# Performance work log

Measured on AMD Instinct MI355X. Metric: run time of the kernel, lower is better.

## Reference

```python
import jax, jax.numpy as jnp
import numpy as np

BIG_NEG = -1000000000.0
B, N, X, D = 16, 32, 36, 2048
H = 512

def setup_inputs() -> dict:
    key = jax.random.key(0)
    ks = jax.random.split(key, 16)
    inp = {
        'fc_feats_target': jax.random.normal(ks[0], (B, 1, D), jnp.float32),
        'fc_feats_distr': jax.random.normal(ks[1], (B, N, D), jnp.float32),
        'att_feats_target': jax.random.normal(ks[2], (B, 1, X, D), jnp.float32),
        'att_feats_distr': jax.random.normal(ks[3], (B, N, X, D), jnp.float32),
        'att_masks_target': jax.random.randint(ks[4], (B, 1, X), 0, 2, jnp.int32),
        'att_masks_distr': jax.random.randint(ks[5], (B, N, X), 0, 2, jnp.int32),
        # scorer MLP params: Linear(2D->H), Linear(H->1)
        'W1': jax.random.normal(ks[6], (2 * D, H), jnp.float32) * 0.02,
        'b1': jnp.zeros((H,), jnp.float32),
        'W2': jax.random.normal(ks[7], (H, 1), jnp.float32) * 0.02,
        'b2': jnp.zeros((1,), jnp.float32),
        # bilinear weight, initialized to identity as in the module
        'Wbil': jnp.eye(D, dtype=jnp.float32),
        # object_scorer MLP params
        'oW1': jax.random.normal(ks[8], (2 * D, H), jnp.float32) * 0.02,
        'ob1': jnp.zeros((H,), jnp.float32),
        'oW2': jax.random.normal(ks[9], (H, 1), jnp.float32) * 0.02,
        'ob2': jnp.zeros((1,), jnp.float32),
    }
    return inp

def _mlp(x, W1, b1, W2, b2):
    h = jax.nn.relu(x @ W1 + b1)
    return (h @ W2 + b2)[..., 0]  # squeeze(-1)

def reference(fc_feats_target, fc_feats_distr, att_feats_target, att_feats_distr,
              att_masks_target, att_masks_distr,
              W1, b1, W2, b2, Wbil, oW1, ob1, oW2, ob2):
    # base scorer on global (fc) features
    ft = jnp.broadcast_to(fc_feats_target, fc_feats_distr.shape)  # [B,N,D]
    cat_feats = jnp.concatenate([ft, fc_feats_distr], axis=-1)    # [B,N,2D]
    scores = _mlp(cat_feats, W1, b1, W2, b2)                      # [B,N]

    # bilinear compatibility: einsum('bixd,biye,de->bixy') with target broadcast over i
    tproj = jnp.einsum('bxd,de->bxe', att_feats_target[:, 0], Wbil)        # [B,X,D]
    inners = jnp.einsum('bxd,biyd->bixy', tproj, att_feats_distr)          # [B,N,X,Y]

    mask_outer = (att_masks_target[:, 0][:, None, :, None]
                  * att_masks_distr[:, :, None, :])                        # [B,N,X,Y]
    inners = jnp.where(mask_outer > 0, inners, BIG_NEG)

    target_weights = jax.nn.softmax(jnp.max(inners, axis=3), axis=-1)      # [B,N,X]
    distr_weights = jax.nn.softmax(jnp.max(inners, axis=2), axis=-1)       # [B,N,Y]

    target_feats = jnp.einsum('bxd,bix->bid', att_feats_target[:, 0], target_weights)
    distr_feats = jnp.einsum('biyd,biy->bid', att_feats_distr, distr_weights)

    cat_att = jnp.concatenate([target_feats, distr_feats], axis=-1)        # [B,N,2D]
    scores = scores + _mlp(cat_att, oW1, ob1, oW2, ob2)

    return jax.nn.log_softmax(scores, axis=-1)  # [B,N]
```

## Files before the change

### kernel.cpp

```cpp
#include <hip/hip_runtime.h>
#include <math.h>

#define D_   2048
#define H_   512
#define K2D  4096
#define X_   36
#define NCOL 1152

#define Z_MLP 16
#define Z_TP  4
#define Z_S   2

#define O_A   0u
#define O_B   4718592u
#define O_TW  6815744u
#define O_DW  6834176u
#define O_SB  6852608u
#define O_SO  6853120u

#define SP_PLANE 663552u

typedef __attribute__((ext_vector_type(8))) short bf8_t;
typedef __attribute__((ext_vector_type(4))) float f4_t;

__device__ __forceinline__ unsigned short f2bf(float f) {
  unsigned u = __float_as_uint(f);
  unsigned r = u + 0x7FFFu + ((u >> 16) & 1u);
  return (unsigned short)(r >> 16);
}
__device__ __forceinline__ float bf2f(unsigned short h) {
  return __uint_as_float(((unsigned)h) << 16);
}

#define TSTR 40

__global__ __launch_bounds__(256, 1) void gemm_mfma(
    const float* __restrict__ A, const float* __restrict__ A2,
    const float* __restrict__ Bm, float* __restrict__ Cpart,
    int M, int N, int K, int kchunk, int amode)
{
  __shared__ __align__(16) unsigned short AsH[128 * TSTR], AsL[128 * TSTR];
  __shared__ __align__(16) unsigned short BsH[128 * TSTR], BsL[128 * TSTR];
  const int t  = threadIdx.x;
  const int m0 = blockIdx.y << 7;
  const int n0 = blockIdx.x << 7;
  const int k0 = blockIdx.z * kchunk;
  const int kend = k0 + kchunk;
  const int w  = t >> 6;
  const int ln = t & 15;
  const int qd = (t >> 4) & 3;
  const int wm = (w >> 1) << 6;
  const int wn = (w & 1) << 6;

  f4_t acc[4][4];
  #pragma unroll
  for (int i = 0; i < 4; i++)
    #pragma unroll
    for (int j = 0; j < 4; j++) acc[i][j] = (f4_t)0.f;

  for (int kb = k0; kb < kend; kb += 32) {
    __syncthreads();
    if (t < 128) {
      int col = t;
      float v[32];
      #pragma unroll
      for (int k = 0; k < 32; k++)
        v[k] = Bm[(size_t)(kb + k) * N + n0 + col];
      __align__(16) unsigned short hb[32], lb[32];
      #pragma unroll
      for (int k = 0; k < 32; k++) {
        unsigned short h = f2bf(v[k]);
        hb[k] = h;
        lb[k] = f2bf(v[k] - bf2f(h));
      }
      #pragma unroll
      for (int j = 0; j < 4; j++) {
        *(bf8_t*)&BsH[col * TSTR + j * 8] = *(bf8_t*)&hb[j * 8];
        *(bf8_t*)&BsL[col * TSTR + j * 8] = *(bf8_t*)&lb[j * 8];
      }
    } else {
      int row = t - 128;
      int gr  = m0 + row;
      float4 va[8];
      #pragma unroll
      for (int j = 0; j < 8; j++) va[j] = make_float4(0.f, 0.f, 0.f, 0.f);
      if (gr < M) {
        #pragma unroll
        for (int j = 0; j < 8; j++) {
          int gk = kb + (j << 2);
          const float* src;
          if (amode == 0) src = A + (size_t)gr * K + gk;
          else src = (gk < 2048) ? (A  + ((size_t)(gr >> 5) << 11) + gk)
                                 : (A2 + ((size_t)gr << 11) + (gk - 2048));
          va[j] = *(const float4*)src;
        }
      }
      __align__(16) unsigned short hb[32], lb[32];
      #pragma unroll
      for (int j = 0; j < 8; j++) {
        float x0 = va[j].x, x1 = va[j].y, x2 = va[j].z, x3 = va[j].w;
        unsigned short h0 = f2bf(x0), h1 = f2bf(x1), h2 = f2bf(x2), h3 = f2bf(x3);
        hb[4*j+0] = h0; hb[4*j+1] = h1; hb[4*j+2] = h2; hb[4*j+3] = h3;
        lb[4*j+0] = f2bf(x0 - bf2f(h0));
        lb[4*j+1] = f2bf(x1 - bf2f(h1));
        lb[4*j+2] = f2bf(x2 - bf2f(h2));
        lb[4*j+3] = f2bf(x3 - bf2f(h3));
      }
      #pragma unroll
      for (int j = 0; j < 4; j++) {
        *(bf8_t*)&AsH[row * TSTR + j * 8] = *(bf8_t*)&hb[j * 8];
        *(bf8_t*)&AsL[row * TSTR + j * 8] = *(bf8_t*)&lb[j * 8];
      }
    }
    __syncthreads();
    bf8_t ah[4], al[4], bh[4], bl[4];
    #pragma unroll
    for (int fm = 0; fm < 4; fm++) {
      int r = (wm + (fm << 4) + ln) * TSTR + (qd << 3);
      ah[fm] = *(const bf8_t*)&AsH[r];
      al[fm] = *(const bf8_t*)&AsL[r];
    }
    #pragma unroll
    for (int fn = 0; fn < 4; fn++) {
      int r = (wn + (fn << 4) + ln) * TSTR + (qd << 3);
      bh[fn] = *(const bf8_t*)&BsH[r];
      bl[fn] = *(const bf8_t*)&BsL[r];
    }
    #pragma unroll
    for (int fm = 0; fm < 4; fm++)
      #pragma unroll
      for (int fn = 0; fn < 4; fn++) {
        acc[fm][fn] = __builtin_amdgcn_mfma_f32_16x16x32_bf16(ah[fm], bh[fn], acc[fm][fn], 0, 0, 0);
        acc[fm][fn] = __builtin_amdgcn_mfma_f32_16x16x32_bf16(ah[fm], bl[fn], acc[fm][fn], 0, 0, 0);
        acc[fm][fn] = __builtin_amdgcn_mfma_f32_16x16x32_bf16(al[fm], bh[fn], acc[fm][fn], 0, 0, 0);
      }
  }
  float* Cz = Cpart + (size_t)blockIdx.z * M * N;
  #pragma unroll
  for (int fm = 0; fm < 4; fm++) {
    #pragma unroll
    for (int reg = 0; reg < 4; reg++) {
      int gr = m0 + wm + (fm << 4) + (qd << 2) + reg;
      if (gr < M) {
        #pragma unroll
        for (int fn = 0; fn < 4; fn++)
          Cz[(size_t)gr * N + n0 + wn + (fn << 4) + ln] = acc[fm][fn][reg];
      }
    }
  }
}

__global__ __launch_bounds__(256) void reduce_tp(
    const float* __restrict__ tpp, float* __restrict__ tproj)
{
  int idx = blockIdx.x * 256 + threadIdx.x;
  const float4* p = (const float4*)tpp;
  float4 a = p[idx];
  #pragma unroll
  for (int z = 1; z < Z_TP; z++) {
    float4 b = p[idx + (size_t)z * 294912];
    a.x += b.x; a.y += b.y; a.z += b.z; a.w += b.w;
  }
  ((float4*)tproj)[idx] = a;
}

__global__ __launch_bounds__(256, 1) void sgemm36_mfma(
    const float* __restrict__ tproj, const float* __restrict__ attd,
    float* __restrict__ Spart, int kchunk)
{
  __shared__ __align__(16) unsigned short AsH[48 * TSTR], AsL[48 * TSTR];
  __shared__ __align__(16) unsigned short BsH[128 * TSTR], BsL[128 * TSTR];
  const int t  = threadIdx.x;
  const int n0 = blockIdx.x << 7;
  const int b  = blockIdx.y;
  const int k0 = blockIdx.z * kchunk;
  const int kend = k0 + kchunk;
  const int w  = t >> 6;
  const int ln = t & 15;
  const int qd = (t >> 4) & 3;
  const float* Ab = tproj + (size_t)b * X_ * D_;
  const float* Bb = attd  + (size_t)b * NCOL * D_;

  f4_t acc[3][2];
  #pragma unroll
  for (int i = 0; i < 3; i++)
    #pragma unroll
    for (int j = 0; j < 2; j++) acc[i][j] = (f4_t)0.f;

  for (int kb = k0; kb < kend; kb += 32) {
    __syncthreads();
    if (t < 128) {
      int col = t;
      float4 v[8];
      #pragma unroll
      for (int j = 0; j < 8; j++)
        v[j] = *(const float4*)(Bb + (size_t)(n0 + col) * D_ + kb + (j << 2));
      __align__(16) unsigned short hb[32], lb[32];
      #pragma unroll
      for (int j = 0; j < 8; j++) {
        float x0 = v[j].x, x1 = v[j].y, x2 = v[j].z, x3 = v[j].w;
        unsigned short h0 = f2bf(x0), h1 = f2bf(x1), h2 = f2bf(x2), h3 = f2bf(x3);
        hb[4*j+0] = h0; hb[4*j+1] = h1; hb[4*j+2] = h2; hb[4*j+3] = h3;
        lb[4*j+0] = f2bf(x0 - bf2f(h0));
        lb[4*j+1] = f2bf(x1 - bf2f(h1));
        lb[4*j+2] = f2bf(x2 - bf2f(h2));
        lb[4*j+3] = f2bf(x3 - bf2f(h3));
      }
      #pragma unroll
      for (int j = 0; j < 4; j++) {
        *(bf8_t*)&BsH[col * TSTR + j * 8] = *(bf8_t*)&hb[j * 8];
        *(bf8_t*)&BsL[col * TSTR + j * 8] = *(bf8_t*)&lb[j * 8];
      }
    } else if (t < 176) {
      int row = t - 128;
      float4 v[8];
      #pragma unroll
      for (int j = 0; j < 8; j++) v[j] = make_float4(0.f, 0.f, 0.f, 0.f);
      if (row < X_) {
        #pragma unroll
        for (int j = 0; j < 8; j++)
          v[j] = *(const float4*)(Ab + (size_t)row * D_ + kb + (j << 2));
      }
      __align__(16) unsigned short hb[32], lb[32];
      #pragma unroll
      for (int j = 0; j < 8; j++) {
        float x0 = v[j].x, x1 = v[j].y, x2 = v[j].z, x3 = v[j].w;
        unsigned short h0 = f2bf(x0), h1 = f2bf(x1), h2 = f2bf(x2), h3 = f2bf(x3);
        hb[4*j+0] = h0; hb[4*j+1] = h1; hb[4*j+2] = h2; hb[4*j+3] = h3;
        lb[4*j+0] = f2bf(x0 - bf2f(h0));
        lb[4*j+1] = f2bf(x1 - bf2f(h1));
        lb[4*j+2] = f2bf(x2 - bf2f(h2));
        lb[4*j+3] = f2bf(x3 - bf2f(h3));
      }
      #pragma unroll
      for (int j = 0; j < 4; j++) {
        *(bf8_t*)&AsH[row * TSTR + j * 8] = *(bf8_t*)&hb[j * 8];
        *(bf8_t*)&AsL[row * TSTR + j * 8] = *(bf8_t*)&lb[j * 8];
      }
    }
    __syncthreads();
    bf8_t ah[3], al[3], bh[2], bl[2];
    #pragma unroll
    for (int fm = 0; fm < 3; fm++) {
      int r = ((fm << 4) + ln) * TSTR + (qd << 3);
      ah[fm] = *(const bf8_t*)&AsH[r];
      al[fm] = *(const bf8_t*)&AsL[r];
    }
    #pragma unroll
    for (int fn = 0; fn < 2; fn++) {
      int r = ((w << 5) + (fn << 4) + ln) * TSTR + (qd << 3);
      bh[fn] = *(const bf8_t*)&BsH[r];
      bl[fn] = *(const bf8_t*)&BsL[r];
    }
    #pragma unroll
    for (int fm = 0; fm < 3; fm++)
      #pragma unroll
      for (int fn = 0; fn < 2; fn++) {
        acc[fm][fn] = __builtin_amdgcn_mfma_f32_16x16x32_bf16(ah[fm], bh[fn], acc[fm][fn], 0, 0, 0);
        acc[fm][fn] = __builtin_amdgcn_mfma_f32_16x16x32_bf16(ah[fm], bl[fn], acc[fm][fn], 0, 0, 0);
        acc[fm][fn] = __builtin_amdgcn_mfma_f32_16x16x32_bf16(al[fm], bh[fn], acc[fm][fn], 0, 0, 0);
      }
  }
  float* Sz = Spart + (size_t)blockIdx.z * SP_PLANE + (size_t)b * X_ * NCOL;
  #pragma unroll
  for (int fm = 0; fm < 3; fm++) {
    #pragma unroll
    for (int reg = 0; reg < 4; reg++) {
      int x = (fm << 4) + (qd << 2) + reg;
      if (x < X_) {
        #pragma unroll
        for (int fn = 0; fn < 2; fn++) {
          int col = n0 + (w << 5) + (fn << 4) + ln;
          Sz[(size_t)x * NCOL + col] = acc[fm][fn][reg];
        }
      }
    }
  }
}

__global__ __launch_bounds__(256) void mlp_tail_z(
    const float* __restrict__ hp, const float* __restrict__ b1,
    const float* __restrict__ w2, const float* __restrict__ b2,
    float* __restrict__ out)
{
  int row = blockIdx.x;
  int t   = threadIdx.x;
  float v = 0.f;
  #pragma unroll
  for (int q = 0; q < 2; q++) {
    int h = t + (q << 8);
    float s = 0.f;
    #pragma unroll
    for (int z = 0; z < Z_MLP; z++)
      s += hp[(size_t)z * (H_ * 512) + (size_t)row * H_ + h];
    s += b1[h];
    v += fmaxf(s, 0.f) * w2[h];
  }
  #pragma unroll
  for (int off = 32; off > 0; off >>= 1) v += __shfl_down(v, off, 64);
  __shared__ float red[4];
  if ((t & 63) == 0) red[t >> 6] = v;
  __syncthreads();
  if (t == 0) out[row] = red[0] + red[1] + red[2] + red[3] + b2[0];
}

__global__ __launch_bounds__(64) void attn_weights(
    const float* __restrict__ Spart, const int* __restrict__ amt,
    const int* __restrict__ amd, float* __restrict__ tw, float* __restrict__ dw)
{
  __shared__ float Sm[36 * 37];
  __shared__ int   mtv[36], mdv[36];
  __shared__ float mrow[36], mcol[36];
  int bi = blockIdx.x;
  int b  = bi >> 5;
  int i  = bi & 31;
  int t  = threadIdx.x;
  if (t < 36) { mtv[t] = amt[b * 36 + t]; mdv[t] = amd[bi * 36 + t]; }
  __syncthreads();
  for (int f = t; f < 324; f += 64) {
    int x  = f / 9;
    int yq = (f - x * 9) << 2;
    size_t o = (((size_t)b * X_ + x) * NCOL + i * 36 + yq) >> 2;
    const float4* p = (const float4*)Spart;
    float4 v = p[o];
    #pragma unroll
    for (int z = 1; z < Z_S; z++) {
      float4 w2 = p[o + ((size_t)z * SP_PLANE >> 2)];
      v.x += w2.x; v.y += w2.y; v.z += w2.z; v.w += w2.w;
    }
    float* dst = &Sm[x * 37 + yq];
    bool mx = (mtv[x] != 0);
    dst[0] = (mx && mdv[yq + 0] != 0) ? v.x : -1e9f;
    dst[1] = (mx && mdv[yq + 1] != 0) ? v.y : -1e9f;
    dst[2] = (mx && mdv[yq + 2] != 0) ? v.z : -1e9f;
    dst[3] = (mx && mdv[yq + 3] != 0) ? v.w : -1e9f;
  }
  __syncthreads();
  if (t < 36) {
    float r = -INFINITY, c = -INFINITY;
    for (int k = 0; k < 36; k++) {
      r = fmaxf(r, Sm[t * 37 + k]);
      c = fmaxf(c, Sm[k * 37 + t]);
    }
    mrow[t] = r; mcol[t] = c;
  }
  __syncthreads();
  {
    float v = (t < 36) ? mrow[t] : -INFINITY;
    float m = v;
    #pragma unroll
    for (int off = 32; off > 0; off >>= 1) m = fmaxf(m, __shfl_xor(m, off, 64));
    float e = (t < 36) ? expf(v - m) : 0.f;
    float s = e;
    #pragma unroll
    for (int off = 32; off > 0; off >>= 1) s += __shfl_xor(s, off, 64);
    if (t < 36) tw[bi * 36 + t] = e / s;
  }
  {
    float v = (t < 36) ? mcol[t] : -INFINITY;
    float m = v;
    #pragma unroll
    for (int off = 32; off > 0; off >>= 1) m = fmaxf(m, __shfl_xor(m, off, 64));
    float e = (t < 36) ? expf(v - m) : 0.f;
    float s = e;
    #pragma unroll
    for (int off = 32; off > 0; off >>= 1) s += __shfl_xor(s, off, 64);
    if (t < 36) dw[bi * 36 + t] = e / s;
  }
}

__global__ __launch_bounds__(256) void wfeats(
    const float* __restrict__ attt, const float* __restrict__ attd,
    const float* __restrict__ tw, const float* __restrict__ dw,
    float* __restrict__ cat)
{
  __shared__ float twl[36], dwl[36];
  int bi = blockIdx.x, b = bi >> 5, t = threadIdx.x;
  if (t < 36) { twl[t] = tw[bi * 36 + t]; dwl[t] = dw[bi * 36 + t]; }
  __syncthreads();
  const float4* at4 = (const float4*)(attt + (size_t)b * X_ * D_);
  const float4* ad4 = (const float4*)(attd + (size_t)bi * X_ * D_);
  float4 t0 = make_float4(0, 0, 0, 0), t1 = t0, d0 = t0, d1 = t0;
  for (int x = 0; x < 36; x++) {
    float wt = twl[x], wd = dwl[x];
    float4 a  = at4[x * 512 + t];
    float4 a2 = at4[x * 512 + t + 256];
    float4 e  = ad4[x * 512 + t];
    float4 e2 = ad4[x * 512 + t + 256];
    t0.x = fmaf(wt, a.x, t0.x);  t0.y = fmaf(wt, a.y, t0.y);
    t0.z = fmaf(wt, a.z, t0.z);  t0.w = fmaf(wt, a.w, t0.w);
    t1.x = fmaf(wt, a2.x, t1.x); t1.y = fmaf(wt, a2.y, t1.y);
    t1.z = fmaf(wt, a2.z, t1.z); t1.w = fmaf(wt, a2.w, t1.w);
    d0.x = fmaf(wd, e.x, d0.x);  d0.y = fmaf(wd, e.y, d0.y);
    d0.z = fmaf(wd, e.z, d0.z);  d0.w = fmaf(wd, e.w, d0.w);
    d1.x = fmaf(wd, e2.x, d1.x); d1.y = fmaf(wd, e2.y, d1.y);
    d1.z = fmaf(wd, e2.z, d1.z); d1.w = fmaf(wd, e2.w, d1.w);
  }
  float4* c4 = (float4*)(cat + (size_t)bi * K2D);
  c4[t] = t0; c4[t + 256] = t1; c4[512 + t] = d0; c4[512 + t + 256] = d1;
}

__global__ __launch_bounds__(64) void lsm(
    const float* __restrict__ sb, const float* __restrict__ so,
    float* __restrict__ out)
{
  int b = blockIdx.x, t = threadIdx.x;
  float s = (t < 32) ? sb[b * 32 + t] + so[b * 32 + t] : -INFINITY;
  float m = s;
  #pragma unroll
  for (int off = 32; off > 0; off >>= 1) m = fmaxf(m, __shfl_xor(m, off, 64));
  float e = (t < 32) ? expf(s - m) : 0.f;
  float sum = e;
  #pragma unroll
  for (int off = 32; off > 0; off >>= 1) sum += __shfl_xor(sum, off, 64);
  if (t < 32) out[b * 32 + t] = s - m - logf(sum);
}

extern "C" void kernel_launch(void* const* d_in, const int* in_sizes, int n_in,
                              void* d_out, int out_size, void* d_ws, size_t ws_size,
                              hipStream_t stream)
{
  const float* fc_t  = (const float*)d_in[0];
  const float* fc_d  = (const float*)d_in[1];
  const float* att_t = (const float*)d_in[2];
  const float* att_d = (const float*)d_in[3];
  const int*   am_t  = (const int*)d_in[4];
  const int*   am_d  = (const int*)d_in[5];
  const float* W1    = (const float*)d_in[6];
  const float* b1    = (const float*)d_in[7];
  const float* W2    = (const float*)d_in[8];
  const float* b2    = (const float*)d_in[9];
  const float* Wbil  = (const float*)d_in[10];
  const float* oW1   = (const float*)d_in[11];
  const float* ob1   = (const float*)d_in[12];
  const float* oW2   = (const float*)d_in[13];
  const float* ob2   = (const float*)d_in[14];
  float* ws  = (float*)d_ws;
  float* out = (float*)d_out;

  gemm_mfma<<<dim3(4, 4, Z_MLP), 256, 0, stream>>>(fc_t, fc_d, W1, ws + O_A,
                                                   512, 512, 4096, 4096 / Z_MLP, 1);
  mlp_tail_z<<<512, 256, 0, stream>>>(ws + O_A, b1, W2, b2, ws + O_SB);
  gemm_mfma<<<dim3(16, 5, Z_TP), 256, 0, stream>>>(att_t, nullptr, Wbil, ws + O_A,
                                                   576, 2048, 2048, 2048 / Z_TP, 0);
  reduce_tp<<<1152, 256, 0, stream>>>(ws + O_A, ws + O_B);
  sgemm36_mfma<<<dim3(9, 16, Z_S), 256, 0, stream>>>(ws + O_B, att_d, ws + O_A,
                                                     2048 / Z_S);
  attn_weights<<<512, 64, 0, stream>>>(ws + O_A, am_t, am_d, ws + O_TW, ws + O_DW);
  wfeats<<<512, 256, 0, stream>>>(att_t, att_d, ws + O_TW, ws + O_DW, ws + O_B);
  gemm_mfma<<<dim3(4, 4, Z_MLP), 256, 0, stream>>>(ws + O_B, nullptr, oW1, ws + O_A,
                                                   512, 512, 4096, 4096 / Z_MLP, 0);
  mlp_tail_z<<<512, 256, 0, stream>>>(ws + O_A, ob1, oW2, ob2, ws + O_SO);
  lsm<<<16, 64, 0, stream>>>(ws + O_SB, ws + O_SO, out);
}
```

Before: 416.5 us.

## Shrink GEMM tiles, raise split-K, prefetch next tile, fuse attention weights with feature pooling

```diff
diff --git a/kernel.cpp b/kernel.cpp
--- a/kernel.cpp
+++ b/kernel.cpp
@@ -7,16 +7,14 @@
 #define X_   36
 #define NCOL 1152
 
-#define Z_MLP 16
-#define Z_TP  4
-#define Z_S   2
+#define Z_MLP 32
+#define Z_TP  8
+#define Z_S   4
 
 #define O_A   0u
-#define O_B   4718592u
-#define O_TW  6815744u
-#define O_DW  6834176u
-#define O_SB  6852608u
-#define O_SO  6853120u
+#define O_B   9437184u
+#define O_SB  11534336u
+#define O_SO  11534848u
 
 #define SP_PLANE 663552u
 
@@ -34,102 +32,97 @@
 
 #define TSTR 40
 
-__global__ __launch_bounds__(256, 1) void gemm_mfma(
+__device__ __forceinline__ void cvt8(unsigned short* Hp, unsigned short* Lp,
+                                     float4 a, float4 b) {
+  __align__(16) unsigned short h[8], l[8];
+  float x[8] = {a.x, a.y, a.z, a.w, b.x, b.y, b.z, b.w};
+  #pragma unroll
+  for (int j = 0; j < 8; j++) {
+    h[j] = f2bf(x[j]);
+    l[j] = f2bf(x[j] - bf2f(h[j]));
+  }
+  *(bf8_t*)Hp = *(bf8_t*)&h[0];
+  *(bf8_t*)Lp = *(bf8_t*)&l[0];
+}
+
+__global__ __launch_bounds__(256, 4) void gemm_mfma64(
     const float* __restrict__ A, const float* __restrict__ A2,
     const float* __restrict__ Bm, float* __restrict__ Cpart,
     int M, int N, int K, int kchunk, int amode)
 {
-  __shared__ __align__(16) unsigned short AsH[128 * TSTR], AsL[128 * TSTR];
-  __shared__ __align__(16) unsigned short BsH[128 * TSTR], BsL[128 * TSTR];
+  __shared__ __align__(16) unsigned short AsH[64 * TSTR], AsL[64 * TSTR];
+  __shared__ __align__(16) unsigned short BsH[64 * TSTR], BsL[64 * TSTR];
   const int t  = threadIdx.x;
-  const int m0 = blockIdx.y << 7;
-  const int n0 = blockIdx.x << 7;
+  const int m0 = blockIdx.y << 6;
+  const int n0 = blockIdx.x << 6;
   const int k0 = blockIdx.z * kchunk;
   const int kend = k0 + kchunk;
   const int w  = t >> 6;
   const int ln = t & 15;
   const int qd = (t >> 4) & 3;
-  const int wm = (w >> 1) << 6;
-  const int wn = (w & 1) << 6;
-
-  f4_t acc[4][4];
-  #pragma unroll
-  for (int i = 0; i < 4; i++)
-    #pragma unroll
-    for (int j = 0; j < 4; j++) acc[i][j] = (f4_t)0.f;
+  const int wm = (w >> 1) << 5;
+  const int wn = (w & 1) << 5;
+  const int a_row = t >> 2;
+  const int a_kq  = (t & 3) << 3;
+  const int b_col = t & 63;
+  const int b_kq  = (t >> 6) << 3;
+
+  f4_t acc[2][2];
+  #pragma unroll
+  for (int i = 0; i < 2; i++)
+    #pragma unroll
+    for (int j = 0; j < 2; j++) acc[i][j] = (f4_t)0.f;
+
+  float4 pa0, pa1;
+  float  pb[8];
+
+  auto loadA = [&](int kb) {
+    int gr = m0 + a_row;
+    int gk = kb + a_kq;
+    pa0 = make_float4(0.f, 0.f, 0.f, 0.f);
+    pa1 = pa0;
+    if (gr < M) {
+      const float* src;
+      if (amode == 0) src = A + (size_t)gr * K + gk;
+      else src = (gk < 2048) ? (A  + ((size_t)(gr >> 5) << 11) + gk)
+                             : (A2 + ((size_t)gr << 11) + (gk - 2048));
+      pa0 = *(const float4*)src;
+      pa1 = *(const float4*)(src + 4);
+    }
+  };
+  auto loadB = [&](int kb) {
+    #pragma unroll
+    for (int j = 0; j < 8; j++)
+      pb[j] = Bm[(size_t)(kb + b_kq + j) * N + n0 + b_col];
+  };
+
+  loadA(k0); loadB(k0);
 
   for (int kb = k0; kb < kend; kb += 32) {
     __syncthreads();
-    if (t < 128) {
-      int col = t;
-      float v[32];
-      #pragma unroll
-      for (int k = 0; k < 32; k++)
-        v[k] = Bm[(size_t)(kb + k) * N + n0 + col];
-      __align__(16) unsigned short hb[32], lb[32];
-      #pragma unroll
-      for (int k = 0; k < 32; k++) {
-        unsigned short h = f2bf(v[k]);
-        hb[k] = h;
-        lb[k] = f2bf(v[k] - bf2f(h));
-      }
-      #pragma unroll
-      for (int j = 0; j < 4; j++) {
-        *(bf8_t*)&BsH[col * TSTR + j * 8] = *(bf8_t*)&hb[j * 8];
-        *(bf8_t*)&BsL[col * TSTR + j * 8] = *(bf8_t*)&lb[j * 8];
-      }
-    } else {
-      int row = t - 128;
-      int gr  = m0 + row;
-      float4 va[8];
-      #pragma unroll
-      for (int j = 0; j < 8; j++) va[j] = make_float4(0.f, 0.f, 0.f, 0.f);
-      if (gr < M) {
-        #pragma unroll
-        for (int j = 0; j < 8; j++) {
-          int gk = kb + (j << 2);
-          const float* src;
-          if (amode == 0) src = A + (size_t)gr * K + gk;
-          else src = (gk < 2048) ? (A  + ((size_t)(gr >> 5) << 11) + gk)
-                                 : (A2 + ((size_t)gr << 11) + (gk - 2048));
-          va[j] = *(const float4*)src;
-        }
-      }
-      __align__(16) unsigned short hb[32], lb[32];
-      #pragma unroll
-      for (int j = 0; j < 8; j++) {
-        float x0 = va[j].x, x1 = va[j].y, x2 = va[j].z, x3 = va[j].w;
-        unsigned short h0 = f2bf(x0), h1 = f2bf(x1), h2 = f2bf(x2), h3 = f2bf(x3);
-        hb[4*j+0] = h0; hb[4*j+1] = h1; hb[4*j+2] = h2; hb[4*j+3] = h3;
-        lb[4*j+0] = f2bf(x0 - bf2f(h0));
-        lb[4*j+1] = f2bf(x1 - bf2f(h1));
-        lb[4*j+2] = f2bf(x2 - bf2f(h2));
-        lb[4*j+3] = f2bf(x3 - bf2f(h3));
-      }
-      #pragma unroll
-      for (int j = 0; j < 4; j++) {
-        *(bf8_t*)&AsH[row * TSTR + j * 8] = *(bf8_t*)&hb[j * 8];
-        *(bf8_t*)&AsL[row * TSTR + j * 8] = *(bf8_t*)&lb[j * 8];
-      }
-    }
+    cvt8(&AsH[a_row * TSTR + a_kq], &AsL[a_row * TSTR + a_kq], pa0, pa1);
+    cvt8(&BsH[b_col * TSTR + b_kq], &BsL[b_col * TSTR + b_kq],
+         make_float4(pb[0], pb[1], pb[2], pb[3]),
+         make_float4(pb[4], pb[5], pb[6], pb[7]));
     __syncthreads();
-    bf8_t ah[4], al[4], bh[4], bl[4];
-    #pragma unroll
-    for (int fm = 0; fm < 4; fm++) {
+    if (kb + 32 < kend) { loadA(kb + 32); loadB(kb + 32); }
+    bf8_t ah[2], al[2], bh[2], bl[2];
+    #pragma unroll
+    for (int fm = 0; fm < 2; fm++) {
       int r = (wm + (fm << 4) + ln) * TSTR + (qd << 3);
       ah[fm] = *(const bf8_t*)&AsH[r];
       al[fm] = *(const bf8_t*)&AsL[r];
     }
     #pragma unroll
-    for (int fn = 0; fn < 4; fn++) {
+    for (int fn = 0; fn < 2; fn++) {
       int r = (wn + (fn << 4) + ln) * TSTR + (qd << 3);
       bh[fn] = *(const bf8_t*)&BsH[r];
       bl[fn] = *(const bf8_t*)&BsL[r];
     }
     #pragma unroll
-    for (int fm = 0; fm < 4; fm++)
+    for (int fm = 0; fm < 2; fm++)
       #pragma unroll
-      for (int fn = 0; fn < 4; fn++) {
+      for (int fn = 0; fn < 2; fn++) {
         acc[fm][fn] = __builtin_amdgcn_mfma_f32_16x16x32_bf16(ah[fm], bh[fn], acc[fm][fn], 0, 0, 0);
         acc[fm][fn] = __builtin_amdgcn_mfma_f32_16x16x32_bf16(ah[fm], bl[fn], acc[fm][fn], 0, 0, 0);
         acc[fm][fn] = __builtin_amdgcn_mfma_f32_16x16x32_bf16(al[fm], bh[fn], acc[fm][fn], 0, 0, 0);
@@ -137,13 +130,13 @@
   }
   float* Cz = Cpart + (size_t)blockIdx.z * M * N;
   #pragma unroll
-  for (int fm = 0; fm < 4; fm++) {
+  for (int fm = 0; fm < 2; fm++) {
     #pragma unroll
     for (int reg = 0; reg < 4; reg++) {
       int gr = m0 + wm + (fm << 4) + (qd << 2) + reg;
       if (gr < M) {
         #pragma unroll
-        for (int fn = 0; fn < 4; fn++)
+        for (int fn = 0; fn < 2; fn++)
           Cz[(size_t)gr * N + n0 + wn + (fn << 4) + ln] = acc[fm][fn][reg];
       }
     }
@@ -164,14 +157,14 @@
   ((float4*)tproj)[idx] = a;
 }
 
-__global__ __launch_bounds__(256, 1) void sgemm36_mfma(
+__global__ __launch_bounds__(256, 4) void sgemm36_mfma(
     const float* __restrict__ tproj, const float* __restrict__ attd,
     float* __restrict__ Spart, int kchunk)
 {
   __shared__ __align__(16) unsigned short AsH[48 * TSTR], AsL[48 * TSTR];
-  __shared__ __align__(16) unsigned short BsH[128 * TSTR], BsL[128 * TSTR];
+  __shared__ __align__(16) unsigned short BsH[64 * TSTR], BsL[64 * TSTR];
   const int t  = threadIdx.x;
-  const int n0 = blockIdx.x << 7;
+  const int n0 = blockIdx.x << 6;
   const int b  = blockIdx.y;
   const int k0 = blockIdx.z * kchunk;
   const int kend = k0 + kchunk;
@@ -180,86 +173,59 @@
   const int qd = (t >> 4) & 3;
   const float* Ab = tproj + (size_t)b * X_ * D_;
   const float* Bb = attd  + (size_t)b * NCOL * D_;
-
-  f4_t acc[3][2];
-  #pragma unroll
-  for (int i = 0; i < 3; i++)
-    #pragma unroll
-    for (int j = 0; j < 2; j++) acc[i][j] = (f4_t)0.f;
+  const int a_row = t >> 2;
+  const int a_kq  = (t & 3) << 3;
+  const int b_col = t & 63;
+  const int b_kq  = (t >> 6) << 3;
+
+  f4_t acc[3];
+  #pragma unroll
+  for (int i = 0; i < 3; i++) acc[i] = (f4_t)0.f;
+
+  float4 pa0, pa1, pb0, pb1;
+
+  auto loadA = [&](int kb) {
+    pa0 = make_float4(0.f, 0.f, 0.f, 0.f);
+    pa1 = pa0;
+    if (a_row < X_) {
+      const float* src = Ab + (size_t)a_row * D_ + kb + a_kq;
+      pa0 = *(const float4*)src;
+      pa1 = *(const float4*)(src + 4);
+    }
+  };
+  auto loadB = [&](int kb) {
+    const float* src = Bb + (size_t)(n0 + b_col) * D_ + kb + b_kq;
+    pb0 = *(const float4*)src;
+    pb1 = *(const float4*)(src + 4);
+  };
+
+  loadA(k0); loadB(k0);
 
   for (int kb = k0; kb < kend; kb += 32) {
     __syncthreads();
-    if (t < 128) {
-      int col = t;
-      float4 v[8];
-      #pragma unroll
-      for (int j = 0; j < 8; j++)
-        v[j] = *(const float4*)(Bb + (size_t)(n0 + col) * D_ + kb + (j << 2));
-      __align__(16) unsigned short hb[32], lb[32];
-      #pragma unroll
-      for (int j = 0; j < 8; j++) {
-        float x0 = v[j].x, x1 = v[j].y, x2 = v[j].z, x3 = v[j].w;
-        unsigned short h0 = f2bf(x0), h1 = f2bf(x1), h2 = f2bf(x2), h3 = f2bf(x3);
-        hb[4*j+0] = h0; hb[4*j+1] = h1; hb[4*j+2] = h2; hb[4*j+3] = h3;
-        lb[4*j+0] = f2bf(x0 - bf2f(h0));
-        lb[4*j+1] = f2bf(x1 - bf2f(h1));
-        lb[4*j+2] = f2bf(x2 - bf2f(h2));
-        lb[4*j+3] = f2bf(x3 - bf2f(h3));
-      }
-      #pragma unroll
-      for (int j = 0; j < 4; j++) {
-        *(bf8_t*)&BsH[col * TSTR + j * 8] = *(bf8_t*)&hb[j * 8];
-        *(bf8_t*)&BsL[col * TSTR + j * 8] = *(bf8_t*)&lb[j * 8];
-      }
-    } else if (t < 176) {
-      int row = t - 128;
-      float4 v[8];
-      #pragma unroll
-      for (int j = 0; j < 8; j++) v[j] = make_float4(0.f, 0.f, 0.f, 0.f);
-      if (row < X_) {
-        #pragma unroll
-        for (int j = 0; j < 8; j++)
-          v[j] = *(const float4*)(Ab + (size_t)row * D_ + kb + (j << 2));
-      }
-      __align__(16) unsigned short hb[32], lb[32];
-      #pragma unroll
-      for (int j = 0; j < 8; j++) {
-        float x0 = v[j].x, x1 = v[j].y, x2 = v[j].z, x3 = v[j].w;
-        unsigned short h0 = f2bf(x0), h1 = f2bf(x1), h2 = f2bf(x2), h3 = f2bf(x3);
-        hb[4*j+0] = h0; hb[4*j+1] = h1; hb[4*j+2] = h2; hb[4*j+3] = h3;
-        lb[4*j+0] = f2bf(x0 - bf2f(h0));
-        lb[4*j+1] = f2bf(x1 - bf2f(h1));
-        lb[4*j+2] = f2bf(x2 - bf2f(h2));
-        lb[4*j+3] = f2bf(x3 - bf2f(h3));
-      }
-      #pragma unroll
-      for (int j = 0; j < 4; j++) {
-        *(bf8_t*)&AsH[row * TSTR + j * 8] = *(bf8_t*)&hb[j * 8];
-        *(bf8_t*)&AsL[row * TSTR + j * 8] = *(bf8_t*)&lb[j * 8];
-      }
-    }
+    if (a_row < 48)
+      cvt8(&AsH[a_row * TSTR + a_kq], &AsL[a_row * TSTR + a_kq], pa0, pa1);
+    cvt8(&BsH[b_col * TSTR + b_kq], &BsL[b_col * TSTR + b_kq], pb0, pb1);
     __syncthreads();
-    bf8_t ah[3], al[3], bh[2], bl[2];
+    if (kb + 32 < kend) { loadA(kb + 32); loadB(kb + 32); }
+    bf8_t ah[3], al[3], bh, bl;
     #pragma unroll
     for (int fm = 0; fm < 3; fm++) {
       int r = ((fm << 4) + ln) * TSTR + (qd << 3);
       ah[fm] = *(const bf8_t*)&AsH[r];
       al[fm] = *(const bf8_t*)&AsL[r];
     }
-    #pragma unroll
-    for (int fn = 0; fn < 2; fn++) {
-      int r = ((w << 5) + (fn << 4) + ln) * TSTR + (qd << 3);
-      bh[fn] = *(const bf8_t*)&BsH[r];
-      bl[fn] = *(const bf8_t*)&BsL[r];
-    }
-    #pragma unroll
-    for (int fm = 0; fm < 3; fm++)
-      #pragma unroll
-      for (int fn = 0; fn < 2; fn++) {
-        acc[fm][fn] = __builtin_amdgcn_mfma_f32_16x16x32_bf16(ah[fm], bh[fn], acc[fm][fn], 0, 0, 0);
-        acc[fm][fn] = __builtin_amdgcn_mfma_f32_16x16x32_bf16(ah[fm], bl[fn], acc[fm][fn], 0, 0, 0);
-        acc[fm][fn] = __builtin_amdgcn_mfma_f32_16x16x32_bf16(al[fm], bh[fn], acc[fm][fn], 0, 0, 0);
-      }
+    {
+      int r = ((w << 4) + ln) * TSTR + (qd << 3);
+      bh = *(const bf8_t*)&BsH[r];
+      bl = *(const bf8_t*)&BsL[r];
+    }
+    #pragma unroll
+    for (int fm = 0; fm < 3; fm++) {
+      acc[fm] = __builtin_amdgcn_mfma_f32_16x16x32_bf16(ah[fm], bh, acc[fm], 0, 0, 0);
+      acc[fm] = __builtin_amdgcn_mfma_f32_16x16x32_bf16(ah[fm], bl, acc[fm], 0, 0, 0);
+      acc[fm] = __builtin_amdgcn_mfma_f32_16x16x32_bf16(al[fm], bh, acc[fm], 0, 0, 0);
+    }
   }
   float* Sz = Spart + (size_t)blockIdx.z * SP_PLANE + (size_t)b * X_ * NCOL;
   #pragma unroll
@@ -267,13 +233,8 @@
     #pragma unroll
     for (int reg = 0; reg < 4; reg++) {
       int x = (fm << 4) + (qd << 2) + reg;
-      if (x < X_) {
-        #pragma unroll
-        for (int fn = 0; fn < 2; fn++) {
-          int col = n0 + (w << 5) + (fn << 4) + ln;
-          Sz[(size_t)x * NCOL + col] = acc[fm][fn][reg];
-        }
-      }
+      if (x < X_)
+        Sz[(size_t)x * NCOL + n0 + (w << 4) + ln] = acc[fm][reg];
     }
   }
 }
@@ -304,20 +265,21 @@
   if (t == 0) out[row] = red[0] + red[1] + red[2] + red[3] + b2[0];
 }
 
-__global__ __launch_bounds__(64) void attn_weights(
+__global__ __launch_bounds__(256) void attn_fused(
     const float* __restrict__ Spart, const int* __restrict__ amt,
-    const int* __restrict__ amd, float* __restrict__ tw, float* __restrict__ dw)
+    const int* __restrict__ amd, const float* __restrict__ attt,
+    const float* __restrict__ attd, float* __restrict__ cat)
 {
   __shared__ float Sm[36 * 37];
   __shared__ int   mtv[36], mdv[36];
-  __shared__ float mrow[36], mcol[36];
+  __shared__ float mrow[36], mcol[36], twl[36], dwl[36];
   int bi = blockIdx.x;
   int b  = bi >> 5;
   int i  = bi & 31;
   int t  = threadIdx.x;
   if (t < 36) { mtv[t] = amt[b * 36 + t]; mdv[t] = amd[bi * 36 + t]; }
   __syncthreads();
-  for (int f = t; f < 324; f += 64) {
+  for (int f = t; f < 324; f += 256) {
     int x  = f / 9;
     int yq = (f - x * 9) << 2;
     size_t o = (((size_t)b * X_ + x) * NCOL + i * 36 + yq) >> 2;
@@ -325,8 +287,8 @@
     float4 v = p[o];
     #pragma unroll
     for (int z = 1; z < Z_S; z++) {
-      float4 w2 = p[o + ((size_t)z * SP_PLANE >> 2)];
-      v.x += w2.x; v.y += w2.y; v.z += w2.z; v.w += w2.w;
+      float4 wv = p[o + ((size_t)z * SP_PLANE >> 2)];
+      v.x += wv.x; v.y += wv.y; v.z += wv.z; v.w += wv.w;
     }
     float* dst = &Sm[x * 37 + yq];
     bool mx = (mtv[x] != 0);
@@ -345,7 +307,7 @@
     mrow[t] = r; mcol[t] = c;
   }
   __syncthreads();
-  {
+  if (t < 64) {
     float v = (t < 36) ? mrow[t] : -INFINITY;
     float m = v;
     #pragma unroll
@@ -354,29 +316,19 @@
     float s = e;
     #pragma unroll
     for (int off = 32; off > 0; off >>= 1) s += __shfl_xor(s, off, 64);
-    if (t < 36) tw[bi * 36 + t] = e / s;
-  }
-  {
-    float v = (t < 36) ? mcol[t] : -INFINITY;
+    if (t < 36) twl[t] = e / s;
+  } else if (t < 128) {
+    int l = t - 64;
+    float v = (l < 36) ? mcol[l] : -INFINITY;
     float m = v;
     #pragma unroll
     for (int off = 32; off > 0; off >>= 1) m = fmaxf(m, __shfl_xor(m, off, 64));
-    float e = (t < 36) ? expf(v - m) : 0.f;
+    float e = (l < 36) ? expf(v - m) : 0.f;
     float s = e;
     #pragma unroll
     for (int off = 32; off > 0; off >>= 1) s += __shfl_xor(s, off, 64);
-    if (t < 36) dw[bi * 36 + t] = e / s;
-  }
-}
-
-__global__ __launch_bounds__(256) void wfeats(
-    const float* __restrict__ attt, const float* __restrict__ attd,
-    const float* __restrict__ tw, const float* __restrict__ dw,
-    float* __restrict__ cat)
-{
-  __shared__ float twl[36], dwl[36];
-  int bi = blockIdx.x, b = bi >> 5, t = threadIdx.x;
-  if (t < 36) { twl[t] = tw[bi * 36 + t]; dwl[t] = dw[bi * 36 + t]; }
+    if (l < 36) dwl[l] = e / s;
+  }
   __syncthreads();
   const float4* at4 = (const float4*)(attt + (size_t)b * X_ * D_);
   const float4* ad4 = (const float4*)(attd + (size_t)bi * X_ * D_);
@@ -438,18 +390,17 @@
   float* ws  = (float*)d_ws;
   float* out = (float*)d_out;
 
-  gemm_mfma<<<dim3(4, 4, Z_MLP), 256, 0, stream>>>(fc_t, fc_d, W1, ws + O_A,
-                                                   512, 512, 4096, 4096 / Z_MLP, 1);
+  gemm_mfma64<<<dim3(8, 8, Z_MLP), 256, 0, stream>>>(fc_t, fc_d, W1, ws + O_A,
+                                                     512, 512, 4096, 4096 / Z_MLP, 1);
   mlp_tail_z<<<512, 256, 0, stream>>>(ws + O_A, b1, W2, b2, ws + O_SB);
-  gemm_mfma<<<dim3(16, 5, Z_TP), 256, 0, stream>>>(att_t, nullptr, Wbil, ws + O_A,
-                                                   576, 2048, 2048, 2048 / Z_TP, 0);
+  gemm_mfma64<<<dim3(32, 9, Z_TP), 256, 0, stream>>>(att_t, nullptr, Wbil, ws + O_A,
+                                                     576, 2048, 2048, 2048 / Z_TP, 0);
   reduce_tp<<<1152, 256, 0, stream>>>(ws + O_A, ws + O_B);
-  sgemm36_mfma<<<dim3(9, 16, Z_S), 256, 0, stream>>>(ws + O_B, att_d, ws + O_A,
-                                                     2048 / Z_S);
-  attn_weights<<<512, 64, 0, stream>>>(ws + O_A, am_t, am_d, ws + O_TW, ws + O_DW);
-  wfeats<<<512, 256, 0, stream>>>(att_t, att_d, ws + O_TW, ws + O_DW, ws + O_B);
-  gemm_mfma<<<dim3(4, 4, Z_MLP), 256, 0, stream>>>(ws + O_B, nullptr, oW1, ws + O_A,
-                                                   512, 512, 4096, 4096 / Z_MLP, 0);
+  sgemm36_mfma<<<dim3(18, 16, Z_S), 256, 0, stream>>>(ws + O_B, att_d, ws + O_A,
+                                                      2048 / Z_S);
+  attn_fused<<<512, 256, 0, stream>>>(ws + O_A, am_t, am_d, att_t, att_d, ws + O_B);
+  gemm_mfma64<<<dim3(8, 8, Z_MLP), 256, 0, stream>>>(ws + O_B, nullptr, oW1, ws + O_A,
+                                                     512, 512, 4096, 4096 / Z_MLP, 0);
   mlp_tail_z<<<512, 256, 0, stream>>>(ws + O_A, ob1, oW2, ob2, ws + O_SO);
   lsm<<<16, 64, 0, stream>>>(ws + O_SB, ws + O_SO, out);
 }
```

Result: faster. 389.3 us (-6.5%).
